# Optimization experiments

Hardware: AMD Instinct MI355X
Metric: run time of the kernel (lower is better)

## Reference

```python
import jax, jax.numpy as jnp
import numpy as np


def setup_inputs() -> dict:
    key = jax.random.key(0)
    k1, k2 = jax.random.split(key)
    B, N, M = 16, 4096, 4096
    xyz1 = jax.random.normal(k1, (B, N, 3), dtype=jnp.float32)
    xyz2 = jax.random.normal(k2, (B, M, 3), dtype=jnp.float32)
    return {"xyz1": xyz1, "xyz2": xyz2}


def reference(xyz1, xyz2):
    sq1 = jnp.sum(xyz1 * xyz1, axis=-1)            # [B, N]
    sq2 = jnp.sum(xyz2 * xyz2, axis=-1)            # [B, M]
    inner = jnp.einsum('bnd,bmd->bnm', xyz1, xyz2)  # [B, N, M]
    d = sq1[:, :, None] + sq2[:, None, :] - 2.0 * inner
    dist1 = jnp.min(d, axis=2)  # nearest in xyz2 for each point of xyz1, [B, N]
    dist2 = jnp.min(d, axis=1)  # nearest in xyz1 for each point of xyz2, [B, M]
    return (jnp.mean(dist1), jnp.mean(dist2))
```

## Files before the change

### kernel.cpp

```cpp
#include <hip/hip_runtime.h>
#include <float.h>

#define BATCH  16
#define NPTS   4096
#define TOTALP (BATCH * NPTS)
#define NQ     (2 * TOTALP)

typedef _Float16 half8  __attribute__((ext_vector_type(8)));
typedef float    f32x16 __attribute__((ext_vector_type(16)));

#define ONE2 0x3C003C00u

__device__ __forceinline__ unsigned enc(float f)
{
    unsigned b = __float_as_uint(f);
    return (b & 0x80000000u) ? ~b : (b | 0x80000000u);
}
__device__ __forceinline__ float dec(unsigned k)
{
    return (k & 0x80000000u) ? __uint_as_float(k & 0x7FFFFFFFu)
                             : __uint_as_float(~k);
}

__device__ __forceinline__ unsigned pk(_Float16 lo, _Float16 hi)
{
    const unsigned a = (unsigned)__builtin_bit_cast(unsigned short, lo);
    const unsigned b = (unsigned)__builtin_bit_cast(unsigned short, hi);
    return a | (b << 16);
}

__device__ __forceinline__ float min16(const f32x16& d, float acc)
{
    const float m1 = fminf(fminf(d[0],  d[1]),  d[2]);
    const float m2 = fminf(fminf(d[3],  d[4]),  d[5]);
    const float m3 = fminf(fminf(d[6],  d[7]),  d[8]);
    const float m4 = fminf(fminf(d[9],  d[10]), d[11]);
    const float m5 = fminf(fminf(d[12], d[13]), d[14]);
    const float m6 = fminf(fminf(m1, m2), m3);
    const float m7 = fminf(fminf(m4, m5), d[15]);
    return fminf(fminf(m6, m7), acc);
}

__global__ __launch_bounds__(256) void prep_kernel(
    const float* __restrict__ xyz1, const float* __restrict__ xyz2,
    uint4* __restrict__ packQ, uint4* __restrict__ planes,
    unsigned* __restrict__ keys, float* __restrict__ out)
{
    const int i = blockIdx.x * 256 + threadIdx.x;
    if (i == 0) { out[0] = 0.0f; out[1] = 0.0f; }
    keys[i] = 0xFFFFFFFFu;

    const float* src = (i < TOTALP) ? xyz1 : xyz2;
    const int p = i & (TOTALP - 1);
    const float x = src[3 * p + 0];
    const float y = src[3 * p + 1];
    const float z = src[3 * p + 2];
    const float sq = x * x + y * y + z * z;
    const _Float16 sh = (_Float16)sq;
    const _Float16 sl = (_Float16)(sq - (float)sh);

    const _Float16 vxh = (_Float16)x, vyh = (_Float16)y, vzh = (_Float16)z;
    const _Float16 vxl = (_Float16)(x - (float)vxh);
    const _Float16 vyl = (_Float16)(y - (float)vyh);
    const _Float16 vzl = (_Float16)(z - (float)vzh);
    planes[i]      = make_uint4(pk(vxh, vyh), pk(vzh, vxh),
                                pk(vyh, vzh), pk(vxl, vyl));
    planes[NQ + i] = make_uint4(pk(vzl, vxl), pk(vyl, vzl),
                                ONE2,         pk(sh, sl));

    const float ux = -2.0f * x, uy = -2.0f * y, uz = -2.0f * z;
    const _Float16 uxh = (_Float16)ux, uyh = (_Float16)uy, uzh = (_Float16)uz;
    const _Float16 uxl = (_Float16)(ux - (float)uxh);
    const _Float16 uyl = (_Float16)(uy - (float)uyh);
    const _Float16 uzl = (_Float16)(uz - (float)uzh);
    packQ[i] = make_uint4(pk(uxh, uyh), pk(uzh, uxl), pk(uyl, uzl), pk(sh, sl));
}

__global__ __launch_bounds__(256) void chamfer_flip2(
    const uint4* __restrict__ packQ, const uint4* __restrict__ planes,
    unsigned* __restrict__ keys)
{
    const int blk = blockIdx.x;
    const int ch  = blk & 7;
    const int qc  = (blk >> 3) & 7;
    const int b   = (blk >> 6) & 15;
    const int dir = blk >> 10;

    const int lane = threadIdx.x & 63;
    const int wv   = threadIdx.x >> 6;
    const int n32  = lane & 31;
    const int half = lane >> 5;

    const int qbase = dir * TOTALP + b * NPTS + qc * 512 + wv * 128;
    half8 bfrag[4];
#pragma unroll
    for (int qf = 0; qf < 4; ++qf) {
        const uint4 d = packQ[qbase + qf * 32 + n32];
        const uint4 u = half ? make_uint4(d.y, d.z, d.w, ONE2)
                             : make_uint4(d.x, d.y, d.z, d.x);
        bfrag[qf] = __builtin_bit_cast(half8, u);
    }

    float acc[4];
#pragma unroll
    for (int qf = 0; qf < 4; ++qf) acc[qf] = FLT_MAX;

    f32x16 cz;
#pragma unroll
    for (int r = 0; r < 16; ++r) cz[r] = 0.0f;

    const uint4* __restrict__ ap =
        planes + (size_t)half * NQ + (dir ^ 1) * TOTALP + b * NPTS + ch * 512;

    uint4 cur = ap[n32];
    for (int tile = 0; tile < 16; ++tile) {
        const uint4 nxt = ap[(((tile + 1) & 15) * 32) + n32];
        const half8 af = __builtin_bit_cast(half8, cur);
#pragma unroll
        for (int qf = 0; qf < 4; ++qf) {
            const f32x16 dd = __builtin_amdgcn_mfma_f32_32x32x16_f16(
                af, bfrag[qf], cz, 0, 0, 0);
            acc[qf] = min16(dd, acc[qf]);
        }
        cur = nxt;
    }

#pragma unroll
    for (int qf = 0; qf < 4; ++qf) {
        float v = acc[qf];
        v = fminf(v, __shfl_xor(v, 32));
        if (lane < 32)
            atomicMin(&keys[qbase + qf * 32 + n32], enc(v));
    }
}

__global__ __launch_bounds__(256) void chamfer_final_atomic(
    const unsigned* __restrict__ keys, float* __restrict__ out)
{
    const int dir = blockIdx.x >> 8;
    const int qi  = ((blockIdx.x & 255) << 8) + threadIdx.x;
    const int q   = (dir << 16) + qi;

    float d = dec(keys[q]);

    for (int off = 32; off > 0; off >>= 1)
        d += __shfl_down(d, off);

    __shared__ float wsum[4];
    const int lane = threadIdx.x & 63;
    const int wv   = threadIdx.x >> 6;
    if (lane == 0) wsum[wv] = d;
    __syncthreads();
    if (threadIdx.x == 0) {
        float s = wsum[0] + wsum[1] + wsum[2] + wsum[3];
        atomicAdd(&out[dir], s * (1.0f / (float)TOTALP));
    }
}

__global__ void zero_out_kernel(float* __restrict__ out)
{
    if (threadIdx.x == 0) { out[0] = 0.0f; out[1] = 0.0f; }
}

__global__ __launch_bounds__(256) void chamfer_raw_kernel(
    const float* __restrict__ xyz1, const float* __restrict__ xyz2,
    float* __restrict__ out)
{
    const int blk = blockIdx.x;
    const int dir = blk >> 8;
    const int idx = blk & 255;
    const int b   = idx >> 4;
    const int n0  = (idx & 15) << 8;

    const float* __restrict__ own = (dir == 0 ? xyz1 : xyz2) + (size_t)b * NPTS * 3;
    const float* __restrict__ opp = (dir == 0 ? xyz2 : xyz1) + (size_t)b * NPTS * 3;

    const int n = n0 + threadIdx.x;
    const float ax = own[3 * n + 0];
    const float ay = own[3 * n + 1];
    const float az = own[3 * n + 2];

    float best = FLT_MAX;
    for (int m = 0; m < NPTS; m += 4) {
#pragma unroll
        for (int u = 0; u < 4; ++u) {
            const float px = opp[3 * (m + u) + 0];
            const float py = opp[3 * (m + u) + 1];
            const float pz = opp[3 * (m + u) + 2];
            const float dx = px - ax, dy = py - ay, dz = pz - az;
            float d = dx * dx;
            d = fmaf(dy, dy, d);
            d = fmaf(dz, dz, d);
            best = fminf(best, d);
        }
    }

    float d = best;
    for (int off = 32; off > 0; off >>= 1)
        d += __shfl_down(d, off);

    __shared__ float wsum[4];
    const int lane = threadIdx.x & 63;
    const int wv   = threadIdx.x >> 6;
    if (lane == 0) wsum[wv] = d;
    __syncthreads();
    if (threadIdx.x == 0) {
        float s = wsum[0] + wsum[1] + wsum[2] + wsum[3];
        atomicAdd(&out[dir], s * (1.0f / (float)TOTALP));
    }
}

extern "C" void kernel_launch(void* const* d_in, const int* in_sizes, int n_in,
                              void* d_out, int out_size, void* d_ws, size_t ws_size,
                              hipStream_t stream)
{
    const float* xyz1 = (const float*)d_in[0];
    const float* xyz2 = (const float*)d_in[1];
    float* out = (float*)d_out;

    const size_t keys_bytes  = (size_t)NQ * sizeof(unsigned);
    const size_t packQ_bytes = (size_t)NQ * sizeof(uint4);
    const size_t plane_bytes = (size_t)2 * NQ * sizeof(uint4);

    if (ws_size >= keys_bytes + packQ_bytes + plane_bytes) {
        unsigned* keys   = (unsigned*)d_ws;
        uint4*    packQ  = (uint4*)((char*)d_ws + keys_bytes);
        uint4*    planes = (uint4*)((char*)d_ws + keys_bytes + packQ_bytes);

        prep_kernel<<<NQ / 256, 256, 0, stream>>>(xyz1, xyz2, packQ, planes, keys, out);
        chamfer_flip2<<<2048, 256, 0, stream>>>(packQ, planes, keys);
        chamfer_final_atomic<<<NQ / 256, 256, 0, stream>>>(keys, out);
    } else {
        zero_out_kernel<<<1, 64, 0, stream>>>(out);
        chamfer_raw_kernel<<<512, 256, 0, stream>>>(xyz1, xyz2, out);
    }
}
```

Measured before the change: 94.31 us.

## Fuse min and mean reduction into one kernel with full-row scan per wave

Each wave now owns 32 query points and scans the entire opposite cloud (128 tiles), so the per-query minimum completes in registers. This removes the atomicMin key buffer, its initialization and the separate final reduction kernel, and the wave reduces its sums directly into an atomicAdd. The trade-off is fewer blocks (1024 instead of 2048), only one B fragment per wave so each A load feeds one MFMA instead of four, and longer serial loops per wave.

```diff
diff --git a/kernel.cpp b/kernel.cpp
--- a/kernel.cpp
+++ b/kernel.cpp
@@ -10,17 +10,6 @@
 typedef float    f32x16 __attribute__((ext_vector_type(16)));
 
 #define ONE2 0x3C003C00u
-
-__device__ __forceinline__ unsigned enc(float f)
-{
-    unsigned b = __float_as_uint(f);
-    return (b & 0x80000000u) ? ~b : (b | 0x80000000u);
-}
-__device__ __forceinline__ float dec(unsigned k)
-{
-    return (k & 0x80000000u) ? __uint_as_float(k & 0x7FFFFFFFu)
-                             : __uint_as_float(~k);
-}
 
 __device__ __forceinline__ unsigned pk(_Float16 lo, _Float16 hi)
 {
@@ -44,11 +33,10 @@
 __global__ __launch_bounds__(256) void prep_kernel(
     const float* __restrict__ xyz1, const float* __restrict__ xyz2,
     uint4* __restrict__ packQ, uint4* __restrict__ planes,
-    unsigned* __restrict__ keys, float* __restrict__ out)
+    float* __restrict__ out)
 {
     const int i = blockIdx.x * 256 + threadIdx.x;
     if (i == 0) { out[0] = 0.0f; out[1] = 0.0f; }
-    keys[i] = 0xFFFFFFFFu;
 
     const float* src = (i < TOTALP) ? xyz1 : xyz2;
     const int p = i & (TOTALP - 1);
@@ -76,83 +64,61 @@
     packQ[i] = make_uint4(pk(uxh, uyh), pk(uzh, uxl), pk(uyl, uzl), pk(sh, sl));
 }
 
-__global__ __launch_bounds__(256) void chamfer_flip2(
+__global__ __launch_bounds__(256) void chamfer_fused(
     const uint4* __restrict__ packQ, const uint4* __restrict__ planes,
-    unsigned* __restrict__ keys)
+    float* __restrict__ out)
 {
     const int blk = blockIdx.x;
-    const int ch  = blk & 7;
-    const int qc  = (blk >> 3) & 7;
-    const int b   = (blk >> 6) & 15;
-    const int dir = blk >> 10;
+    const int qc  = blk & 31;
+    const int b   = (blk >> 5) & 15;
+    const int dir = blk >> 9;
 
     const int lane = threadIdx.x & 63;
     const int wv   = threadIdx.x >> 6;
     const int n32  = lane & 31;
     const int half = lane >> 5;
 
-    const int qbase = dir * TOTALP + b * NPTS + qc * 512 + wv * 128;
-    half8 bfrag[4];
-#pragma unroll
-    for (int qf = 0; qf < 4; ++qf) {
-        const uint4 d = packQ[qbase + qf * 32 + n32];
-        const uint4 u = half ? make_uint4(d.y, d.z, d.w, ONE2)
-                             : make_uint4(d.x, d.y, d.z, d.x);
-        bfrag[qf] = __builtin_bit_cast(half8, u);
-    }
-
-    float acc[4];
-#pragma unroll
-    for (int qf = 0; qf < 4; ++qf) acc[qf] = FLT_MAX;
+    const int qbase = dir * TOTALP + b * NPTS + qc * 128 + wv * 32;
+    const uint4 d = packQ[qbase + n32];
+    const uint4 u = half ? make_uint4(d.y, d.z, d.w, ONE2)
+                         : make_uint4(d.x, d.y, d.z, d.x);
+    const half8 bfrag = __builtin_bit_cast(half8, u);
 
     f32x16 cz;
 #pragma unroll
     for (int r = 0; r < 16; ++r) cz[r] = 0.0f;
 
     const uint4* __restrict__ ap =
-        planes + (size_t)half * NQ + (dir ^ 1) * TOTALP + b * NPTS + ch * 512;
-
-    uint4 cur = ap[n32];
-    for (int tile = 0; tile < 16; ++tile) {
-        const uint4 nxt = ap[(((tile + 1) & 15) * 32) + n32];
-        const half8 af = __builtin_bit_cast(half8, cur);
-#pragma unroll
-        for (int qf = 0; qf < 4; ++qf) {
-            const f32x16 dd = __builtin_amdgcn_mfma_f32_32x32x16_f16(
-                af, bfrag[qf], cz, 0, 0, 0);
-            acc[qf] = min16(dd, acc[qf]);
-        }
-        cur = nxt;
-    }
-
-#pragma unroll
-    for (int qf = 0; qf < 4; ++qf) {
-        float v = acc[qf];
-        v = fminf(v, __shfl_xor(v, 32));
-        if (lane < 32)
-            atomicMin(&keys[qbase + qf * 32 + n32], enc(v));
-    }
-}
-
-__global__ __launch_bounds__(256) void chamfer_final_atomic(
-    const unsigned* __restrict__ keys, float* __restrict__ out)
-{
-    const int dir = blockIdx.x >> 8;
-    const int qi  = ((blockIdx.x & 255) << 8) + threadIdx.x;
-    const int q   = (dir << 16) + qi;
-
-    float d = dec(keys[q]);
-
-    for (int off = 32; off > 0; off >>= 1)
-        d += __shfl_down(d, off);
-
+        planes + (size_t)half * NQ + (dir ^ 1) * TOTALP + b * NPTS;
+
+    float acc0 = FLT_MAX, acc1 = FLT_MAX;
+    uint4 c0 = ap[0 * 32 + n32];
+    uint4 c1 = ap[1 * 32 + n32];
+
+    for (int t = 0; t < 128; t += 2) {
+        const uint4 n0 = ap[(((t + 2) & 127) * 32) + n32];
+        const uint4 n1 = ap[(((t + 3) & 127) * 32) + n32];
+        const f32x16 d0 = __builtin_amdgcn_mfma_f32_32x32x16_f16(
+            __builtin_bit_cast(half8, c0), bfrag, cz, 0, 0, 0);
+        const f32x16 d1 = __builtin_amdgcn_mfma_f32_32x32x16_f16(
+            __builtin_bit_cast(half8, c1), bfrag, cz, 0, 0, 0);
+        acc0 = min16(d0, acc0);
+        acc1 = min16(d1, acc1);
+        c0 = n0; c1 = n1;
+    }
+
+    float v = fminf(acc0, acc1);
+    v = fminf(v, __shfl_xor(v, 32));
+    v += __shfl_xor(v, 16);
+    v += __shfl_xor(v, 8);
+    v += __shfl_xor(v, 4);
+    v += __shfl_xor(v, 2);
+    v += __shfl_xor(v, 1);
     __shared__ float wsum[4];
-    const int lane = threadIdx.x & 63;
-    const int wv   = threadIdx.x >> 6;
-    if (lane == 0) wsum[wv] = d;
+    if (lane == 0) wsum[wv] = v;
     __syncthreads();
     if (threadIdx.x == 0) {
-        float s = wsum[0] + wsum[1] + wsum[2] + wsum[3];
+        const float s = wsum[0] + wsum[1] + wsum[2] + wsum[3];
         atomicAdd(&out[dir], s * (1.0f / (float)TOTALP));
     }
 }
@@ -218,18 +184,15 @@
     const float* xyz2 = (const float*)d_in[1];
     float* out = (float*)d_out;
 
-    const size_t keys_bytes  = (size_t)NQ * sizeof(unsigned);
     const size_t packQ_bytes = (size_t)NQ * sizeof(uint4);
     const size_t plane_bytes = (size_t)2 * NQ * sizeof(uint4);
 
-    if (ws_size >= keys_bytes + packQ_bytes + plane_bytes) {
-        unsigned* keys   = (unsigned*)d_ws;
-        uint4*    packQ  = (uint4*)((char*)d_ws + keys_bytes);
-        uint4*    planes = (uint4*)((char*)d_ws + keys_bytes + packQ_bytes);
-
-        prep_kernel<<<NQ / 256, 256, 0, stream>>>(xyz1, xyz2, packQ, planes, keys, out);
-        chamfer_flip2<<<2048, 256, 0, stream>>>(packQ, planes, keys);
-        chamfer_final_atomic<<<NQ / 256, 256, 0, stream>>>(keys, out);
+    if (ws_size >= packQ_bytes + plane_bytes) {
+        uint4* packQ  = (uint4*)d_ws;
+        uint4* planes = (uint4*)((char*)d_ws + packQ_bytes);
+
+        prep_kernel<<<NQ / 256, 256, 0, stream>>>(xyz1, xyz2, packQ, planes, out);
+        chamfer_fused<<<1024, 256, 0, stream>>>(packQ, planes, out);
     } else {
         zero_out_kernel<<<1, 64, 0, stream>>>(out);
         chamfer_raw_kernel<<<512, 256, 0, stream>>>(xyz1, xyz2, out);
```

Result: slower. 101.3 us (+7.5%).
